# Optimization experiments

Measured on AMD Instinct MI355X. Metric: run time of the kernel, lower is better.

## Reference

```python
import jax, jax.numpy as jnp
import numpy as np

H = 4        # nhead
TEMP = 0.1   # temperature
TOP_K = 5
SHAPE_EPS = 1e-5


def _ln(x, g, b):
    m = x.mean(-1, keepdims=True)
    v = ((x - m) ** 2).mean(-1, keepdims=True)
    return (x - m) / jnp.sqrt(v + SHAPE_EPS) * g + b


def _mha(x, Wqkv, bqkv, Wo, bo):
    B, L, D = x.shape
    Dh = D // H
    qkv = x @ Wqkv.T + bqkv                     # [B,L,3D]
    q, k, v = jnp.split(qkv, 3, axis=-1)
    q = q.reshape(B, L, H, Dh)
    k = k.reshape(B, L, H, Dh)
    v = v.reshape(B, L, H, Dh)
    att = jnp.einsum('bqhd,bkhd->bhqk', q, k) * (1.0 / np.sqrt(Dh))
    att = jax.nn.softmax(att, axis=-1)
    o = jnp.einsum('bhqk,bkhd->bqhd', att, v).reshape(B, L, D)
    return o @ Wo.T + bo


def _pattern_encoder(x, cls_token, Wqkv, bqkv, Wo, bo, ln1_g, ln1_b,
                     W1, b1, W2, b2, ln2_g, ln2_b, proj_W, proj_b, proj_g, proj_bb):
    B, L, D = x.shape
    h = jnp.concatenate([jnp.broadcast_to(cls_token, (B, 1, D)), x], axis=1)  # [B,L+1,D]
    for i in range(Wqkv.shape[0]):  # num_layers=2, post-norm (PyTorch default)
        a = _mha(h, Wqkv[i], bqkv[i], Wo[i], bo[i])
        h = _ln(h + a, ln1_g[i], ln1_b[i])
        f = jax.nn.gelu(h @ W1[i].T + b1[i], approximate=False) @ W2[i].T + b2[i]
        h = _ln(h + f, ln2_g[i], ln2_b[i])
    cls_out = h[:, 0, :]
    return _ln(cls_out @ proj_W.T + proj_b, proj_g, proj_bb)  # [B,d_repr]


def _value_encoder(xm, vW1, vb1, v_g, v_b, vW2, vb2):
    hh = _ln(xm @ vW1.T + vb1, v_g, v_b)
    return jax.nn.gelu(hh, approximate=False) @ vW2.T + vb2


def setup_inputs() -> dict:
    B, L, D, DR, N, P, NL = 64, 512, 512, 128, 10000, 96, 2
    key = jax.random.key(0)
    ks = jax.random.split(key, 16)
    sc = 0.02
    inp = {
        'query': jax.random.normal(ks[0], (B, L, D), jnp.float32),
        'memory_keys': jax.random.normal(ks[1], (N, DR), jnp.float32),
        'memory_values': jax.random.normal(ks[2], (N, P, D), jnp.float32),
        'cls_token': jax.random.normal(ks[3], (1, 1, D), jnp.float32) * sc,
        'Wqkv': jax.random.normal(ks[4], (NL, 3 * D, D), jnp.float32) * sc,
        'bqkv': jnp.zeros((NL, 3 * D), jnp.float32),
        'Wo': jax.random.normal(ks[5], (NL, D, D), jnp.float32) * sc,
        'bo': jnp.zeros((NL, D), jnp.float32),
        'ln1_g': jnp.ones((NL, D), jnp.float32),
        'ln1_b': jnp.zeros((NL, D), jnp.float32),
        'W1': jax.random.normal(ks[6], (NL, 2 * D, D), jnp.float32) * sc,
        'b1': jnp.zeros((NL, 2 * D), jnp.float32),
        'W2': jax.random.normal(ks[7], (NL, D, 2 * D), jnp.float32) * sc,
        'b2': jnp.zeros((NL, D), jnp.float32),
        'ln2_g': jnp.ones((NL, D), jnp.float32),
        'ln2_b': jnp.zeros((NL, D), jnp.float32),
        'proj_W': jax.random.normal(ks[8], (DR, D), jnp.float32) * sc,
        'proj_b': jnp.zeros((DR,), jnp.float32),
        'proj_g': jnp.ones((DR,), jnp.float32),
        'proj_bb': jnp.zeros((DR,), jnp.float32),
        'vW1': jax.random.normal(ks[9], (DR, D), jnp.float32) * sc,
        'vb1': jnp.zeros((DR,), jnp.float32),
        'v_g': jnp.ones((DR,), jnp.float32),
        'v_b': jnp.zeros((DR,), jnp.float32),
        'vW2': jax.random.normal(ks[10], (DR, DR), jnp.float32) * sc,
        'vb2': jnp.zeros((DR,), jnp.float32),
        'shape_w': jnp.float32(0.5),
    }
    return inp


def reference(query, memory_keys, memory_values, cls_token, Wqkv, bqkv, Wo, bo,
              ln1_g, ln1_b, W1, b1, W2, b2, ln2_g, ln2_b,
              proj_W, proj_b, proj_g, proj_bb, vW1, vb1, v_g, v_b, vW2, vb2, shape_w):
    q_repr = _pattern_encoder(query, cls_token, Wqkv, bqkv, Wo, bo, ln1_g, ln1_b,
                              W1, b1, W2, b2, ln2_g, ln2_b, proj_W, proj_b, proj_g, proj_bb)
    q_val = _value_encoder(query.mean(axis=1), vW1, vb1, v_g, v_b, vW2, vb2)
    qk = shape_w * q_repr + (1.0 - shape_w) * q_val              # [B,DR]
    # squared euclidean distance, expanded form (same math as sum((a-b)^2))
    d = ((qk ** 2).sum(-1)[:, None]
         - 2.0 * qk @ memory_keys.T
         + (memory_keys ** 2).sum(-1)[None, :])                  # [B,N]
    sim = -d / TEMP
    top_scores, top_idx = jax.lax.top_k(sim, TOP_K)              # [B,K]
    weights = jax.nn.softmax(top_scores, axis=-1)
    retrieved = memory_values[top_idx]                           # [B,K,P,D]
    return retrieved, weights
```

## Files before the change

### kernel.cpp

```cpp
#include <hip/hip_runtime.h>
#include <math.h>

#define B_    64
#define LQ    512
#define LC    513
#define DD    512
#define HH    4
#define DH    128
#define DRr   128
#define NKEYS 10000
#define PP    96
#define TOPK  5
#define MROWS (B_*LC)
#define VTSTRIDE 544

typedef __attribute__((ext_vector_type(8))) short short8v;
typedef __attribute__((ext_vector_type(4))) float f32x4;
typedef __attribute__((ext_vector_type(16))) float f32x16;

static __device__ __forceinline__ float gelu_exact(float x) {
    return 0.5f * x * (1.0f + erff(x * 0.70710678118654752440f));
}

static __device__ __forceinline__ unsigned short f2bf(float x) {
    union { float f; unsigned u; } v; v.f = x;
    unsigned r = v.u + 0x7fff + ((v.u >> 16) & 1);
    return (unsigned short)(r >> 16);
}
static __device__ __forceinline__ float bf2f(unsigned short h) {
    union { float f; unsigned u; } v; v.u = ((unsigned)h) << 16;
    return v.f;
}
static __device__ __forceinline__ void split_bf(float x, unsigned short& hi, unsigned short& lo) {
    hi = f2bf(x);
    lo = f2bf(x - bf2f(hi));
}

static __device__ __forceinline__ int xcd_swz(int orig, int nwg) {
    int xcd = orig & 7;
    int lid = orig >> 3;
    int q = nwg >> 3, r = nwg & 7;
    int base = (xcd < r) ? xcd * (q + 1) : r * (q + 1) + (xcd - r) * q;
    return base + lid;
}

static __device__ __forceinline__ void gload16(const unsigned short* g, unsigned short* l) {
    __builtin_amdgcn_global_load_lds(
        (const __attribute__((address_space(1))) unsigned*)g,
        (__attribute__((address_space(3))) unsigned*)l, 16, 0, 0);
}

__global__ __launch_bounds__(256)
void split_kernel(const float* __restrict__ x, unsigned short* __restrict__ hi,
                  unsigned short* __restrict__ lo, int n4)
{
    int i = blockIdx.x * blockDim.x + threadIdx.x;
    if (i >= n4) return;
    float4 v = ((const float4*)x)[i];
    unsigned short h0,h1,h2,h3,l0,l1,l2,l3;
    split_bf(v.x,h0,l0); split_bf(v.y,h1,l1); split_bf(v.z,h2,l2); split_bf(v.w,h3,l3);
    ((uint2*)hi)[i] = make_uint2((unsigned)h0 | ((unsigned)h1 << 16), (unsigned)h2 | ((unsigned)h3 << 16));
    ((uint2*)lo)[i] = make_uint2((unsigned)l0 | ((unsigned)l1 << 16), (unsigned)l2 | ((unsigned)l3 << 16));
}

__global__ __launch_bounds__(256)
void concat_cls(const float* __restrict__ query, const float* __restrict__ cls,
                float* __restrict__ h, unsigned short* __restrict__ h_hi,
                unsigned short* __restrict__ h_lo)
{
    int row = blockIdx.x * 4 + (threadIdx.x >> 6);
    int lane = threadIdx.x & 63;
    int b = row / LC, r = row - b * LC;
    const float* src = (r == 0) ? (cls + lane * 8)
                                : (query + ((size_t)b * LQ + (r - 1)) * DD + lane * 8);
    float4 v0 = *(const float4*)src;
    float4 v1 = *(const float4*)(src + 4);
    size_t o = (size_t)row * DD + lane * 8;
    *(float4*)(h + o) = v0;
    *(float4*)(h + o + 4) = v1;
    float vv[8] = {v0.x,v0.y,v0.z,v0.w,v1.x,v1.y,v1.z,v1.w};
    unsigned short hs[8], ls[8];
    #pragma unroll
    for (int i = 0; i < 8; i++) split_bf(vv[i], hs[i], ls[i]);
    uint4 hv, lv;
    hv.x = (unsigned)hs[0] | ((unsigned)hs[1] << 16);
    hv.y = (unsigned)hs[2] | ((unsigned)hs[3] << 16);
    hv.z = (unsigned)hs[4] | ((unsigned)hs[5] << 16);
    hv.w = (unsigned)hs[6] | ((unsigned)hs[7] << 16);
    lv.x = (unsigned)ls[0] | ((unsigned)ls[1] << 16);
    lv.y = (unsigned)ls[2] | ((unsigned)ls[3] << 16);
    lv.z = (unsigned)ls[4] | ((unsigned)ls[5] << 16);
    lv.w = (unsigned)ls[6] | ((unsigned)ls[7] << 16);
    *(uint4*)(h_hi + o) = hv;
    *(uint4*)(h_lo + o) = lv;
}

#define BM 128
#define BN 128
#define BK 32

#define MFMA32(a, b, c) __builtin_amdgcn_mfma_f32_32x32x16_bf16(a, b, c, 0, 0, 0)

template<int MODE>
__global__ __launch_bounds__(256)
void gemm3(const unsigned short* __restrict__ Ahi, const unsigned short* __restrict__ Alo,
           const unsigned short* __restrict__ Whi, const unsigned short* __restrict__ Wlo,
           const float* __restrict__ bias, const float* __restrict__ res,
           float* __restrict__ Cf, unsigned short* __restrict__ Chi,
           unsigned short* __restrict__ Clo, unsigned* __restrict__ Vix,
           int M, int N, int K, int NBN)
{
    __shared__ __align__(16) unsigned short POOL[32768];

    const int t = threadIdx.x;
    const int lane = t & 63, w = t >> 6;
    const int wr = w >> 1, wc = w & 1;
    const int wg = xcd_swz(blockIdx.x, gridDim.x);
    const int bm = wg / NBN, bn = wg - bm * NBN;
    const int row0 = bm * BM, col0 = bn * BN;

    const int srow = t >> 2;
    const int sg   = t & 3;
    const int glog = sg ^ (srow & 3);
    int ar0 = row0 + srow;      if (ar0 >= M) ar0 = M - 1;
    int ar1 = row0 + srow + 64; if (ar1 >= M) ar1 = M - 1;
    const size_t aoff0 = (size_t)ar0 * K + glog * 8;
    const size_t aoff1 = (size_t)ar1 * K + glog * 8;
    const size_t boff0 = (size_t)(col0 + srow) * K + glog * 8;
    const size_t boff1 = (size_t)(col0 + srow + 64) * K + glog * 8;
    const int ldso0 = t * 8;
    const int ldso1 = t * 8 + 2048;

    f32x16 acc[2][2];
    #pragma unroll
    for (int m = 0; m < 2; m++)
        #pragma unroll
        for (int n = 0; n < 2; n++)
            #pragma unroll
            for (int i = 0; i < 16; i++) acc[m][n][i] = 0.f;

    const int cl = lane & 31;
    const int kg = lane >> 5;
    const int cl3 = cl & 3;

    const int KT = K / BK;
    gload16(Ahi + aoff0, &POOL[ldso0]);
    gload16(Ahi + aoff1, &POOL[ldso1]);
    gload16(Alo + aoff0, &POOL[4096 + ldso0]);
    gload16(Alo + aoff1, &POOL[4096 + ldso1]);
    gload16(Whi + boff0, &POOL[8192 + ldso0]);
    gload16(Whi + boff1, &POOL[8192 + ldso1]);
    gload16(Wlo + boff0, &POOL[12288 + ldso0]);
    gload16(Wlo + boff1, &POOL[12288 + ldso1]);

    for (int kt = 0; kt < KT; kt++) {
        const int cb = (kt & 1) * 16384;
        const int nb = 16384 - cb;
        if (kt + 1 < KT) {
            const int k0n = (kt + 1) * BK;
            gload16(Ahi + aoff0 + k0n, &POOL[nb + ldso0]);
            gload16(Ahi + aoff1 + k0n, &POOL[nb + ldso1]);
            gload16(Alo + aoff0 + k0n, &POOL[nb + 4096 + ldso0]);
            gload16(Alo + aoff1 + k0n, &POOL[nb + 4096 + ldso1]);
            gload16(Whi + boff0 + k0n, &POOL[nb + 8192 + ldso0]);
            gload16(Whi + boff1 + k0n, &POOL[nb + 8192 + ldso1]);
            gload16(Wlo + boff0 + k0n, &POOL[nb + 12288 + ldso0]);
            gload16(Wlo + boff1 + k0n, &POOL[nb + 12288 + ldso1]);
            asm volatile("s_waitcnt vmcnt(8)" ::: "memory");
        } else {
            asm volatile("s_waitcnt vmcnt(0)" ::: "memory");
        }
        __builtin_amdgcn_s_barrier();
        __builtin_amdgcn_sched_barrier(0);

        #pragma unroll
        for (int ks = 0; ks < 2; ks++) {
            const int blkswz = ((ks * 2 + kg) ^ cl3) * 8;
            short8v ah[2], al[2], bh[2], bl[2];
            #pragma unroll
            for (int m = 0; m < 2; m++) {
                int off = cb + (wr * 64 + m * 32 + cl) * 32 + blkswz;
                ah[m] = *(const short8v*)&POOL[off];
                al[m] = *(const short8v*)&POOL[off + 4096];
            }
            #pragma unroll
            for (int n = 0; n < 2; n++) {
                int off = cb + (wc * 64 + n * 32 + cl) * 32 + blkswz;
                bh[n] = *(const short8v*)&POOL[off + 8192];
                bl[n] = *(const short8v*)&POOL[off + 12288];
            }
            #pragma unroll
            for (int m = 0; m < 2; m++)
                #pragma unroll
                for (int n = 0; n < 2; n++) {
                    acc[m][n] = MFMA32(ah[m], bh[n], acc[m][n]);
                    acc[m][n] = MFMA32(al[m], bh[n], acc[m][n]);
                    acc[m][n] = MFMA32(ah[m], bl[n], acc[m][n]);
                }
        }
        __builtin_amdgcn_s_barrier();
    }

    if (MODE == 3 && col0 >= 1024) {
        const int hh = (col0 - 1024) >> 7;
        unsigned* VS = (unsigned*)POOL;
        const int bb0 = row0 / LC;
        const int bound = (bb0 + 1) * LC;
        const int ddl = t >> 3, j0 = (t & 7) * 16;
        #pragma unroll
        for (int p = 0; p < 4; p++) {
            __syncthreads();
            if (wc == (p >> 1)) {
                const int ccl = col0 + wc * 64 + (p & 1) * 32 + cl;
                const float bcol = bias[ccl];
                #pragma unroll
                for (int m = 0; m < 2; m++) {
                    const int lrb = wr * 64 + m * 32 + 4 * kg;
                    #pragma unroll
                    for (int q = 0; q < 4; q++)
                        #pragma unroll
                        for (int r = 0; r < 4; r++) {
                            float v = ((p & 1) ? acc[m][1][q * 4 + r]
                                               : acc[m][0][q * 4 + r]) + bcol;
                            unsigned short hv, lv;
                            split_bf(v, hv, lv);
                            VS[cl * 129 + lrb + 8 * q + r] =
                                (unsigned)hv | ((unsigned)lv << 16);
                        }
                }
            }
            __syncthreads();
            long long vb0 = (long long)((bb0 * HH + hh) * DH + p * 32 + ddl) * VTSTRIDE
                            - (long long)bb0 * LC;
            long long vb1 = (long long)(((bb0 + 1) * HH + hh) * DH + p * 32 + ddl) * VTSTRIDE
                            - (long long)(bb0 + 1) * LC;
            #pragma unroll
            for (int j = 0; j < 16; j++) {
                int row = row0 + j0 + j;
                if (row < M) {
                    long long vi = (row < bound ? vb0 : vb1) + row;
                    Vix[vi] = VS[ddl * 129 + j0 + j];
                }
            }
        }
        return;
    }

    #pragma unroll
    for (int m = 0; m < 2; m++) {
        const int rb = row0 + wr * 64 + m * 32 + 4 * kg;
        #pragma unroll
        for (int n = 0; n < 2; n++) {
            const int cc = col0 + wc * 64 + n * 32 + cl;
            const float bcol = bias[cc];
            #pragma unroll
            for (int q = 0; q < 4; q++) {
                #pragma unroll
                for (int r = 0; r < 4; r++) {
                    int row = rb + 8 * q + r;
                    if (row < M) {
                        float v = acc[m][n][q * 4 + r] + bcol;
                        if (MODE == 1) v += res[(size_t)row * N + cc];
                        if (MODE == 2) {
                            v = gelu_exact(v);
                            unsigned short hv, lv;
                            split_bf(v, hv, lv);
                            Chi[(size_t)row * N + cc] = hv;
                            Clo[(size_t)row * N + cc] = lv;
                        } else if (MODE == 3) {
                            unsigned short hv, lv;
                            split_bf(v, hv, lv);
                            Chi[(size_t)row * 1024 + cc] = hv;
                            Clo[(size_t)row * 1024 + cc] = lv;
                        } else {
                            Cf[(size_t)row * N + cc] = v;
                        }
                    }
                }
            }
        }
    }
}

#define AQT 64
#define AKT 32
#define NKT2 17
#define MFMA16(a, b, c) __builtin_amdgcn_mfma_f32_16x16x32_bf16(a, b, c, 0, 0, 0)
__global__ __launch_bounds__(256)
void attn_mfma(const unsigned short* __restrict__ qkhi, const unsigned short* __restrict__ qklo,
               const unsigned* __restrict__ vtx,
               unsigned short* __restrict__ ohi, unsigned short* __restrict__ olo)
{
    __shared__ __align__(16) unsigned short SM[24064];
    #define KH(r,d) SM[(r)*136 + (d)]
    #define KL(r,d) SM[4352 + (r)*136 + (d)]
    #define VH(d,k) SM[8704 + (d)*40 + (k)]
    #define VL(d,k) SM[13824 + (d)*40 + (k)]
    #define PH(r,k) SM[18944 + (r)*40 + (k)]
    #define PL(r,k) SM[21504 + (r)*40 + (k)]
    #define OS(r,d) SM[(r)*136 + (d)]

    const int t = threadIdx.x;
    const int lane = t & 63, w = t >> 6;
    const int id = xcd_swz(blockIdx.x, gridDim.x);
    const int qt = id % 9;
    const int hb = id / 9;
    const int h = hb & 3, b = hb >> 2;
    const int q0 = qt * AQT;
    const int c = lane & 15, g = lane >> 4;
    const float SCALE = 0.08838834764831845f;

    short8v qh[4], ql[4];
    {
        int qrow = b * LC + q0 + w * 16 + c;
        if (qrow > MROWS - 1) qrow = MROWS - 1;
        const unsigned short* bh_ = qkhi + (size_t)qrow * 1024 + h * DH;
        const unsigned short* bl_ = qklo + (size_t)qrow * 1024 + h * DH;
        #pragma unroll
        for (int ks = 0; ks < 4; ks++) {
            qh[ks] = *(const short8v*)(bh_ + ks * 32 + g * 8);
            ql[ks] = *(const short8v*)(bl_ + ks * 32 + g * 8);
        }
    }

    float m_r[4], l_r[4];
    #pragma unroll
    for (int r = 0; r < 4; r++) { m_r[r] = -INFINITY; l_r[r] = 0.f; }
    f32x4 acc_o[8];
    #pragma unroll
    for (int n = 0; n < 8; n++) { acc_o[n][0]=0.f; acc_o[n][1]=0.f; acc_o[n][2]=0.f; acc_o[n][3]=0.f; }

    const int skr = t >> 3, skd = (t & 7) * 16;
    const int svd = t >> 1, svk = (t & 1) * 16;
    const unsigned short* kbase  = qkhi + 512 + h * DH + skd;
    const unsigned short* kbasel = qklo + 512 + h * DH + skd;
    const unsigned* vbase = vtx + ((size_t)((b * HH + h) * DH + svd)) * VTSTRIDE + svk;

    short8v rk0, rk1, rl0, rl1;
    uint4 rv0, rv1, rv2, rv3;
    {
        int krow = b * LC + skr; if (krow > MROWS - 1) krow = MROWS - 1;
        const unsigned short* kb  = kbase  + (size_t)krow * 1024;
        const unsigned short* kbl = kbasel + (size_t)krow * 1024;
        rk0 = *(const short8v*)kb;  rk1 = *(const short8v*)(kb + 8);
        rl0 = *(const short8v*)kbl; rl1 = *(const short8v*)(kbl + 8);
        rv0 = *(const uint4*)(vbase);
        rv1 = *(const uint4*)(vbase + 4);
        rv2 = *(const uint4*)(vbase + 8);
        rv3 = *(const uint4*)(vbase + 12);
    }

    for (int kt = 0; kt < NKT2; kt++) {
        __builtin_amdgcn_s_barrier();
        *(short8v*)&KH(skr, skd)     = rk0;
        *(short8v*)&KH(skr, skd + 8) = rk1;
        *(short8v*)&KL(skr, skd)     = rl0;
        *(short8v*)&KL(skr, skd + 8) = rl1;
        {
            uint4 hA, hB, lA, lB;
            hA.x = (rv0.x & 0xffffu) | (rv0.y << 16);
            hA.y = (rv0.z & 0xffffu) | (rv0.w << 16);
            hA.z = (rv1.x & 0xffffu) | (rv1.y << 16);
            hA.w = (rv1.z & 0xffffu) | (rv1.w << 16);
            hB.x = (rv2.x & 0xffffu) | (rv2.y << 16);
            hB.y = (rv2.z & 0xffffu) | (rv2.w << 16);
            hB.z = (rv3.x & 0xffffu) | (rv3.y << 16);
            hB.w = (rv3.z & 0xffffu) | (rv3.w << 16);
            lA.x = (rv0.x >> 16) | (rv0.y & 0xffff0000u);
            lA.y = (rv0.z >> 16) | (rv0.w & 0xffff0000u);
            lA.z = (rv1.x >> 16) | (rv1.y & 0xffff0000u);
            lA.w = (rv1.z >> 16) | (rv1.w & 0xffff0000u);
            lB.x = (rv2.x >> 16) | (rv2.y & 0xffff0000u);
            lB.y = (rv2.z >> 16) | (rv2.w & 0xffff0000u);
            lB.z = (rv3.x >> 16) | (rv3.y & 0xffff0000u);
            lB.w = (rv3.z >> 16) | (rv3.w & 0xffff0000u);
            *(uint4*)&VH(svd, svk)     = hA;
            *(uint4*)&VH(svd, svk + 8) = hB;
            *(uint4*)&VL(svd, svk)     = lA;
            *(uint4*)&VL(svd, svk + 8) = lB;
        }
        if (kt + 1 < NKT2) {
            int krow = b * LC + (kt + 1) * AKT + skr;
            if (krow > MROWS - 1) krow = MROWS - 1;
            const unsigned short* kb  = kbase  + (size_t)krow * 1024;
            const unsigned short* kbl = kbasel + (size_t)krow * 1024;
            rk0 = *(const short8v*)kb;  rk1 = *(const short8v*)(kb + 8);
            rl0 = *(const short8v*)kbl; rl1 = *(const short8v*)(kbl + 8);
            const unsigned* vb = vbase + (kt + 1) * AKT;
            rv0 = *(const uint4*)(vb);
            rv1 = *(const uint4*)(vb + 4);
            rv2 = *(const uint4*)(vb + 8);
            rv3 = *(const uint4*)(vb + 12);
        }
        asm volatile("s_waitcnt lgkmcnt(0)" ::: "memory");
        __builtin_amdgcn_s_barrier();
        __builtin_amdgcn_sched_barrier(0);

        f32x4 s[2];
        s[0][0]=s[0][1]=s[0][2]=s[0][3]=0.f;
        s[1][0]=s[1][1]=s[1][2]=s[1][3]=0.f;
        __builtin_amdgcn_s_setprio(1);
        #pragma unroll
        for (int n = 0; n < 2; n++) {
            #pragma unroll
            for (int ks = 0; ks < 4; ks++) {
                short8v kh = *(const short8v*)&KH(n * 16 + c, ks * 32 + g * 8);
                short8v kl = *(const short8v*)&KL(n * 16 + c, ks * 32 + g * 8);
                s[n] = MFMA16(qh[ks], kh, s[n]);
                s[n] = MFMA16(ql[ks], kh, s[n]);
                s[n] = MFMA16(qh[ks], kl, s[n]);
            }
        }
        __builtin_amdgcn_s_setprio(0);

        #pragma unroll
        for (int n = 0; n < 2; n++) {
            bool oob = (kt * 32 + n * 16 + c) >= LC;
            #pragma unroll
            for (int r = 0; r < 4; r++) {
                float sv = s[n][r] * SCALE;
                s[n][r] = oob ? -INFINITY : sv;
            }
        }

        float alpha[4], p0v[4], p1v[4];
        #pragma unroll
        for (int r = 0; r < 4; r++) {
            float rm = fmaxf(s[0][r], s[1][r]);
            #pragma unroll
            for (int off = 1; off < 16; off <<= 1) rm = fmaxf(rm, __shfl_xor(rm, off));
            float mn = fmaxf(m_r[r], rm);
            float p0 = expf(s[0][r] - mn);
            float p1 = expf(s[1][r] - mn);
            float ts = p0 + p1;
            #pragma unroll
            for (int off = 1; off < 16; off <<= 1) ts += __shfl_xor(ts, off);
            float al = expf(m_r[r] - mn);
            m_r[r] = mn;
            l_r[r] = al * l_r[r] + ts;
            alpha[r] = al;
            p0v[r] = p0; p1v[r] = p1;
        }

        #pragma unroll
        for (int n = 0; n < 8; n++)
            #pragma unroll
            for (int r = 0; r < 4; r++) acc_o[n][r] *= alpha[r];

        #pragma unroll
        for (int r = 0; r < 4; r++) {
            unsigned short ph, pl;
            split_bf(p0v[r], ph, pl);
            PH(w * 16 + g * 4 + r, c) = ph;
            PL(w * 16 + g * 4 + r, c) = pl;
            split_bf(p1v[r], ph, pl);
            PH(w * 16 + g * 4 + r, 16 + c) = ph;
            PL(w * 16 + g * 4 + r, 16 + c) = pl;
        }
        short8v pah = *(const short8v*)&PH(w * 16 + c, g * 8);
        short8v pal = *(const short8v*)&PL(w * 16 + c, g * 8);
        __builtin_amdgcn_s_setprio(1);
        #pragma unroll
        for (int n = 0; n < 8; n++) {
            short8v vh = *(const short8v*)&VH(n * 16 + c, g * 8);
            short8v vl = *(const short8v*)&VL(n * 16 + c, g * 8);
            acc_o[n] = MFMA16(pah, vh, acc_o[n]);
            acc_o[n] = MFMA16(pal, vh, acc_o[n]);
            acc_o[n] = MFMA16(pah, vl, acc_o[n]);
        }
        __builtin_amdgcn_s_setprio(0);
    }

    float inv[4];
    #pragma unroll
    for (int r = 0; r < 4; r++) inv[r] = 1.0f / l_r[r];

    const int orow = t >> 2, oc0 = (t & 3) * 32;
    #pragma unroll
    for (int pass = 0; pass < 2; pass++) {
        __syncthreads();
        #pragma unroll
        for (int n = 0; n < 8; n++)
            #pragma unroll
            for (int r = 0; r < 4; r++) {
                float v = acc_o[n][r] * inv[r];
                unsigned short hv, lv;
                split_bf(v, hv, lv);
                OS(w * 16 + g * 4 + r, n * 16 + c) = pass ? lv : hv;
            }
        __syncthreads();
        int grow = q0 + orow;
        if (grow < LC) {
            unsigned short* dst = (pass ? olo : ohi) + ((size_t)(b * LC + grow)) * DD + h * DH + oc0;
            #pragma unroll
            for (int u = 0; u < 4; u++)
                *(short8v*)(dst + u * 8) = *(const short8v*)&OS(orow, oc0 + u * 8);
        }
    }
    #undef KH
    #undef KL
    #undef VH
    #undef VL
    #undef PH
    #undef PL
    #undef OS
}

__global__ __launch_bounds__(256)
void ln512(const float* __restrict__ X, const float* __restrict__ g,
           const float* __restrict__ bb, float* __restrict__ Y,
           unsigned short* __restrict__ Yhi, unsigned short* __restrict__ Ylo)
{
    int row = blockIdx.x * 4 + (threadIdx.x >> 6);
    int lane = threadIdx.x & 63;
    const float* x = X + (size_t)row * DD + lane * 8;
    float4 v0 = *(const float4*)x;
    float4 v1 = *(const float4*)(x + 4);
    float vv[8] = {v0.x,v0.y,v0.z,v0.w,v1.x,v1.y,v1.z,v1.w};
    float s = 0.f;
    #pragma unroll
    for (int i = 0; i < 8; i++) s += vv[i];
    #pragma unroll
    for (int off = 1; off < 64; off <<= 1) s += __shfl_xor(s, off);
    float mean = s * (1.0f / 512.0f);
    float d[8], s2 = 0.f;
    #pragma unroll
    for (int i = 0; i < 8; i++) { d[i] = vv[i] - mean; s2 += d[i] * d[i]; }
    #pragma unroll
    for (int off = 1; off < 64; off <<= 1) s2 += __shfl_xor(s2, off);
    float var = s2 * (1.0f / 512.0f);
    float rstd = 1.0f / sqrtf(var + 1e-5f);
    float4 g0 = *(const float4*)(g + lane * 8);
    float4 g1 = *(const float4*)(g + lane * 8 + 4);
    float4 b0 = *(const float4*)(bb + lane * 8);
    float4 b1 = *(const float4*)(bb + lane * 8 + 4);
    float gg[8] = {g0.x,g0.y,g0.z,g0.w,g1.x,g1.y,g1.z,g1.w};
    float bv[8] = {b0.x,b0.y,b0.z,b0.w,b1.x,b1.y,b1.z,b1.w};
    float ov[8];
    unsigned short hs[8], ls[8];
    #pragma unroll
    for (int i = 0; i < 8; i++) {
        ov[i] = d[i] * rstd * gg[i] + bv[i];
        split_bf(ov[i], hs[i], ls[i]);
    }
    size_t o = (size_t)row * DD + lane * 8;
    *(float4*)(Y + o)     = make_float4(ov[0], ov[1], ov[2], ov[3]);
    *(float4*)(Y + o + 4) = make_float4(ov[4], ov[5], ov[6], ov[7]);
    uint4 hv, lv;
    hv.x = (unsigned)hs[0] | ((unsigned)hs[1] << 16);
    hv.y = (unsigned)hs[2] | ((unsigned)hs[3] << 16);
    hv.z = (unsigned)hs[4] | ((unsigned)hs[5] << 16);
    hv.w = (unsigned)hs[6] | ((unsigned)hs[7] << 16);
    lv.x = (unsigned)ls[0] | ((unsigned)ls[1] << 16);
    lv.y = (unsigned)ls[2] | ((unsigned)ls[3] << 16);
    lv.z = (unsigned)ls[4] | ((unsigned)ls[5] << 16);
    lv.w = (unsigned)ls[6] | ((unsigned)ls[7] << 16);
    *(uint4*)(Yhi + o) = hv;
    *(uint4*)(Ylo + o) = lv;
}

__global__ __launch_bounds__(128)
void mean_part(const float* __restrict__ query, float* __restrict__ part)
{
    int b = blockIdx.x, ch = blockIdx.y, t = threadIdx.x;
    const float* base = query + ((size_t)b * LQ + ch * 64) * DD + t * 4;
    float ax = 0.f, ay = 0.f, az = 0.f, aw = 0.f;
    for (int l = 0; l < 64; l++) {
        float4 v = *(const float4*)(base + (size_t)l * DD);
        ax += v.x; ay += v.y; az += v.z; aw += v.w;
    }
    *(float4*)(part + ((size_t)(b * 8 + ch)) * DD + t * 4) = make_float4(ax, ay, az, aw);
}

__global__ __launch_bounds__(128)
void mean_fin(const float* __restrict__ part, float* __restrict__ xm)
{
    int b = blockIdx.x, t = threadIdx.x;
    float ax = 0.f, ay = 0.f, az = 0.f, aw = 0.f;
    #pragma unroll
    for (int ch = 0; ch < 8; ch++) {
        float4 v = *(const float4*)(part + ((size_t)(b * 8 + ch)) * DD + t * 4);
        ax += v.x; ay += v.y; az += v.z; aw += v.w;
    }
    *(float4*)(xm + (size_t)b * DD + t * 4) =
        make_float4(ax * (1.f/512.f), ay * (1.f/512.f), az * (1.f/512.f), aw * (1.f/512.f));
}

static __device__ __forceinline__ float block128_sum(float x, float* red, int t) {
    #pragma unroll
    for (int off = 1; off < 64; off <<= 1) x += __shfl_xor(x, off);
    if ((t & 63) == 0) red[t >> 6] = x;
    __syncthreads();
    float r = red[0] + red[1];
    __syncthreads();
    return r;
}

__global__ __launch_bounds__(128)
void proj_ln(const float* __restrict__ h, const float* __restrict__ pW, const float* __restrict__ pb,
             const float* __restrict__ pg, const float* __restrict__ pbb, float* __restrict__ q_repr)
{
    __shared__ float xs[DD];
    __shared__ float red[2];
    int b = blockIdx.x, t = threadIdx.x;
    *(float4*)&xs[t * 4] = *(const float4*)(h + (size_t)(b * LC) * DD + t * 4);
    __syncthreads();
    const float* w = pW + (size_t)t * DD;
    float acc = pb[t];
    for (int k = 0; k < DD; k += 4) {
        float4 a = *(const float4*)&xs[k];
        float4 ww = *(const float4*)(w + k);
        acc += a.x * ww.x + a.y * ww.y + a.z * ww.z + a.w * ww.w;
    }
    float mean = block128_sum(acc, red, t) * (1.f / 128.f);
    float dx = acc - mean;
    float var = block128_sum(dx * dx, red, t) * (1.f / 128.f);
    float rstd = 1.0f / sqrtf(var + 1e-5f);
    q_repr[(size_t)b * DRr + t] = dx * rstd * pg[t] + pbb[t];
}

__global__ __launch_bounds__(128)
void venc(const float* __restrict__ xm, const float* __restrict__ vW1, const float* __restrict__ vb1,
          const float* __restrict__ vg, const float* __restrict__ vb,
          const float* __restrict__ vW2, const float* __restrict__ vb2,
          float* __restrict__ q_val)
{
    __shared__ float xs[DD];
    __shared__ float hg[DRr];
    __shared__ float red[2];
    int b = blockIdx.x, t = threadIdx.x;
    *(float4*)&xs[t * 4] = *(const float4*)(xm + (size_t)b * DD + t * 4);
    __syncthreads();
    const float* w = vW1 + (size_t)t * DD;
    float acc = vb1[t];
    for (int k = 0; k < DD; k += 4) {
        float4 a = *(const float4*)&xs[k];
        float4 ww = *(const float4*)(w + k);
        acc += a.x * ww.x + a.y * ww.y + a.z * ww.z + a.w * ww.w;
    }
    float mean = block128_sum(acc, red, t) * (1.f / 128.f);
    float dx = acc - mean;
    float var = block128_sum(dx * dx, red, t) * (1.f / 128.f);
    float rstd = 1.0f / sqrtf(var + 1e-5f);
    float hn = dx * rstd * vg[t] + vb[t];
    hg[t] = gelu_exact(hn);
    __syncthreads();
    const float* w2 = vW2 + (size_t)t * DRr;
    float acc2 = vb2[t];
    for (int k = 0; k < DRr; k += 4) {
        float4 a = *(const float4*)&hg[k];
        float4 ww = *(const float4*)(w2 + k);
        acc2 += a.x * ww.x + a.y * ww.y + a.z * ww.z + a.w * ww.w;
    }
    q_val[(size_t)b * DRr + t] = acc2;
}

__global__ void combine_qk(const float* __restrict__ qr, const float* __restrict__ qv,
                           const float* __restrict__ swp, float* __restrict__ qk)
{
    int i = blockIdx.x * blockDim.x + threadIdx.x;
    if (i < B_ * DRr) {
        float sw = swp[0];
        qk[i] = sw * qr[i] + (1.f - sw) * qv[i];
    }
}

#define SIMCH 10
__global__ __launch_bounds__(256)
void sim_kernel(const float* __restrict__ qk, const float* __restrict__ mkeys, float* __restrict__ sim)
{
    __shared__ float qs[DRr];
    int b = blockIdx.x, ch = blockIdx.y, t = threadIdx.x;
    if (t < DRr) qs[t] = qk[(size_t)b * DRr + t];
    __syncthreads();
    float qn = 0.f;
    #pragma unroll 8
    for (int i = 0; i < DRr; i++) qn += qs[i] * qs[i];
    int n0 = ch * (NKEYS / SIMCH), n1 = n0 + (NKEYS / SIMCH);
    for (int n = n0 + t; n < n1; n += 256) {
        const float* kr = mkeys + (size_t)n * DRr;
        float dot = 0.f, kn = 0.f;
        #pragma unroll 8
        for (int i = 0; i < DRr; i += 4) {
            float4 kv = *(const float4*)(kr + i);
            dot += qs[i] * kv.x + qs[i + 1] * kv.y + qs[i + 2] * kv.z + qs[i + 3] * kv.w;
            kn  += kv.x * kv.x + kv.y * kv.y + kv.z * kv.z + kv.w * kv.w;
        }
        float d = qn - 2.f * dot + kn;
        sim[(size_t)b * NKEYS + n] = -d / 0.1f;
    }
}

static __device__ __forceinline__ void topk_insert(float* v, int* id, float x, int n) {
    bool better = (x > v[TOPK - 1]) || (x == v[TOPK - 1] && n < id[TOPK - 1]);
    if (better) {
        v[TOPK - 1] = x; id[TOPK - 1] = n;
        #pragma unroll
        for (int k = TOPK - 1; k > 0; k--) {
            bool sw = (v[k] > v[k - 1]) || (v[k] == v[k - 1] && id[k] < id[k - 1]);
            if (!sw) break;
            float tv = v[k]; v[k] = v[k - 1]; v[k - 1] = tv;
            int ti = id[k]; id[k] = id[k - 1]; id[k - 1] = ti;
        }
    }
}

__global__ __launch_bounds__(256)
void topk_kernel(const float* __restrict__ sim, int* __restrict__ topidx, float* __restrict__ wout)
{
    __shared__ float sv[256][TOPK];
    __shared__ int   si[256][TOPK];
    int b = blockIdx.x, t = threadIdx.x;
    float v[TOPK]; int id[TOPK];
    #pragma unroll
    for (int k = 0; k < TOPK; k++) { v[k] = -INFINITY; id[k] = 0x7fffffff; }
    for (int n = t; n < NKEYS; n += 256) {
        topk_insert(v, id, sim[(size_t)b * NKEYS + n], n);
    }
    #pragma unroll
    for (int k = 0; k < TOPK; k++) { sv[t][k] = v[k]; si[t][k] = id[k]; }
    for (int strd = 128; strd >= 1; strd >>= 1) {
        __syncthreads();
        if (t < strd) {
            #pragma unroll
            for (int k = 0; k < TOPK; k++) topk_insert(v, id, sv[t + strd][k], si[t + strd][k]);
            #pragma unroll
            for (int k = 0; k < TOPK; k++) { sv[t][k] = v[k]; si[t][k] = id[k]; }
        }
    }
    if (t == 0) {
        float m = v[0];
        float e[TOPK]; float sum = 0.f;
        #pragma unroll
        for (int k = 0; k < TOPK; k++) { e[k] = expf(v[k] - m); sum += e[k]; }
        #pragma unroll
        for (int k = 0; k < TOPK; k++) {
            wout[(size_t)b * TOPK + k] = e[k] / sum;
            topidx[b * TOPK + k] = id[k];
        }
    }
}

__global__ __launch_bounds__(128)
void gather_kernel(const float* __restrict__ mv, const int* __restrict__ topidx, float* __restrict__ out)
{
    int blk = blockIdx.x;
    int b = blk / (TOPK * PP);
    int rem = blk - b * (TOPK * PP);
    int k = rem / PP;
    int p = rem - k * PP;
    int idx = topidx[b * TOPK + k];
    const float4* src = (const float4*)(mv + ((size_t)idx * PP + p) * DD);
    float4* dst = (float4*)(out + (size_t)blk * DD);
    dst[threadIdx.x] = src[threadIdx.x];
}

extern "C" void kernel_launch(void* const* d_in, const int* in_sizes, int n_in,
                              void* d_out, int out_size, void* d_ws, size_t ws_size,
                              hipStream_t stream) {
    const float* query = (const float*)d_in[0];
    const float* mkeys = (const float*)d_in[1];
    const float* mvals = (const float*)d_in[2];
    const float* cls   = (const float*)d_in[3];
    const float* Wqkv  = (const float*)d_in[4];
    const float* bqkv  = (const float*)d_in[5];
    const float* Wo    = (const float*)d_in[6];
    const float* bo    = (const float*)d_in[7];
    const float* ln1g  = (const float*)d_in[8];
    const float* ln1b  = (const float*)d_in[9];
    const float* W1    = (const float*)d_in[10];
    const float* b1    = (const float*)d_in[11];
    const float* W2    = (const float*)d_in[12];
    const float* b2    = (const float*)d_in[13];
    const float* ln2g  = (const float*)d_in[14];
    const float* ln2b  = (const float*)d_in[15];
    const float* pW    = (const float*)d_in[16];
    const float* pb    = (const float*)d_in[17];
    const float* pg    = (const float*)d_in[18];
    const float* pbb   = (const float*)d_in[19];
    const float* vW1   = (const float*)d_in[20];
    const float* vb1   = (const float*)d_in[21];
    const float* vg    = (const float*)d_in[22];
    const float* vb    = (const float*)d_in[23];
    const float* vW2   = (const float*)d_in[24];
    const float* vb2   = (const float*)d_in[25];
    const float* swp   = (const float*)d_in[26];
    float* out = (float*)d_out;

    float* ws    = (float*)d_ws;
    float* h     = ws;
    float* preln = h + (size_t)MROWS * DD;
    unsigned short* h_hi  = (unsigned short*)(preln + (size_t)MROWS * DD);
    unsigned short* h_lo  = h_hi  + (size_t)MROWS * DD;
    unsigned short* mid_hi = h_lo + (size_t)MROWS * DD;
    unsigned short* mid_lo = mid_hi + (size_t)MROWS * 1024;
    unsigned short* qkhi  = mid_lo + (size_t)MROWS * 1024;
    unsigned short* qklo  = qkhi  + (size_t)MROWS * 1024;
    unsigned* vtx         = (unsigned*)(qklo + (size_t)MROWS * 1024);
    unsigned short* wq_hi = (unsigned short*)(vtx + (size_t)32768 * VTSTRIDE);
    unsigned short* wq_lo = wq_hi + (size_t)2 * 1536 * DD;
    unsigned short* wo_hi = wq_lo + (size_t)2 * 1536 * DD;
    unsigned short* wo_lo = wo_hi + (size_t)2 * DD * DD;
    unsigned short* w1_hi = wo_lo + (size_t)2 * DD * DD;
    unsigned short* w1_lo = w1_hi + (size_t)2 * 1024 * DD;
    unsigned short* w2_hi = w1_lo + (size_t)2 * 1024 * DD;
    unsigned short* w2_lo = w2_hi + (size_t)2 * DD * 1024;
    float* xm   = (float*)(w2_lo + (size_t)2 * DD * 1024);
    float* qval = xm   + (size_t)B_ * DD;
    float* qrep = qval + (size_t)B_ * DRr;
    float* qkc  = qrep + (size_t)B_ * DRr;
    float* simb = qkc  + (size_t)B_ * DRr;
    int*   tidx = (int*)(simb + (size_t)B_ * NKEYS);
    float* mpart = (float*)(tidx + 512);
    (void)ws_size; (void)in_sizes; (void)n_in; (void)out_size;

    {
        int n4;
        n4 = 2 * 1536 * DD / 4;
        split_kernel<<<(n4 + 255) / 256, 256, 0, stream>>>(Wqkv, wq_hi, wq_lo, n4);
        n4 = 2 * DD * DD / 4;
        split_kernel<<<(n4 + 255) / 256, 256, 0, stream>>>(Wo, wo_hi, wo_lo, n4);
        n4 = 2 * 1024 * DD / 4;
        split_kernel<<<(n4 + 255) / 256, 256, 0, stream>>>(W1, w1_hi, w1_lo, n4);
        n4 = 2 * DD * 1024 / 4;
        split_kernel<<<(n4 + 255) / 256, 256, 0, stream>>>(W2, w2_hi, w2_lo, n4);
    }

    concat_cls<<<MROWS / 4, 256, 0, stream>>>(query, cls, h, h_hi, h_lo);

    for (int l = 0; l < 2; l++) {
        const unsigned short* wqh = wq_hi + (size_t)l * 1536 * DD;
        const unsigned short* wql = wq_lo + (size_t)l * 1536 * DD;
        const unsigned short* woh = wo_hi + (size_t)l * DD * DD;
        const unsigned short* wol = wo_lo + (size_t)l * DD * DD;
        const unsigned short* w1h = w1_hi + (size_t)l * 1024 * DD;
        const unsigned short* w1l = w1_lo + (size_t)l * 1024 * DD;
        const unsigned short* w2h = w2_hi + (size_t)l * DD * 1024;
        const unsigned short* w2l = w2_lo + (size_t)l * DD * 1024;
        const float* bq  = bqkv + (size_t)l * 1536;
        const float* bol = bo   + (size_t)l * DD;
        const float* g1  = ln1g + (size_t)l * DD;
        const float* be1 = ln1b + (size_t)l * DD;
        const float* b1l = b1   + (size_t)l * 1024;
        const float* b2l = b2   + (size_t)l * DD;
        const float* g2  = ln2g + (size_t)l * DD;
        const float* be2 = ln2b + (size_t)l * DD;

        gemm3<3><<<257 * 12, 256, 0, stream>>>(h_hi, h_lo, wqh, wql, bq, nullptr,
                                               nullptr, qkhi, qklo, vtx,
                                               MROWS, 1536, DD, 12);
        attn_mfma<<<9 * HH * B_, 256, 0, stream>>>(qkhi, qklo, vtx, h_hi, h_lo);
        gemm3<1><<<257 * 4, 256, 0, stream>>>(h_hi, h_lo, woh, wol, bol, h,
                                              preln, nullptr, nullptr, nullptr,
                                              MROWS, DD, DD, 4);
        ln512<<<MROWS / 4, 256, 0, stream>>>(preln, g1, be1, h, h_hi, h_lo);
        gemm3<2><<<257 * 8, 256, 0, stream>>>(h_hi, h_lo, w1h, w1l, b1l, nullptr,
                                              nullptr, mid_hi, mid_lo, nullptr,
                                              MROWS, 1024, DD, 8);
        gemm3<1><<<257 * 4, 256, 0, stream>>>(mid_hi, mid_lo, w2h, w2l, b2l, h,
                                              preln, nullptr, nullptr, nullptr,
                                              MROWS, DD, 1024, 4);
        ln512<<<MROWS / 4, 256, 0, stream>>>(preln, g2, be2, h, h_hi, h_lo);
    }

    proj_ln<<<B_, 128, 0, stream>>>(h, pW, pb, pg, pbb, qrep);
    mean_part<<<dim3(B_, 8), 128, 0, stream>>>(query, mpart);
    mean_fin<<<B_, 128, 0, stream>>>(mpart, xm);
    venc<<<B_, 128, 0, stream>>>(xm, vW1, vb1, vg, vb, vW2, vb2, qval);
    combine_qk<<<(B_ * DRr + 255) / 256, 256, 0, stream>>>(qrep, qval, swp, qkc);
    sim_kernel<<<dim3(B_, SIMCH), 256, 0, stream>>>(qkc, mkeys, simb);
    topk_kernel<<<B_, 256, 0, stream>>>(simb, tidx, out + (size_t)B_ * TOPK * PP * DD);
    gather_kernel<<<B_ * TOPK * PP, 128, 0, stream>>>(mvals, tidx, out);
}
```

Measured before the change: 2.490 ms.

## Widen GEMM tiles to 128x256 with single-buffered LDS and 4x2 warp tiles

The split-bf16 GEMM output tile grows from 128x128 to 128x256. Each warp now owns all 128 rows and a 64-column slice, so it holds 4x2 accumulators, and grid sizes are halved to match. The LDS double buffer and its async prefetch pipeline are dropped in favour of a single buffer guarded by syncthreads around each load, which cuts LDS so that two blocks can share a CU (launch_bounds 256,2). The aim is more operand reuse per loaded byte and fewer A-matrix reloads, at the cost of global-load latency no longer overlapping MFMA work and higher register pressure.

```diff
diff --git a/kernel.cpp b/kernel.cpp
--- a/kernel.cpp
+++ b/kernel.cpp
@@ -96,13 +96,13 @@
 }
 
 #define BM 128
-#define BN 128
+#define BN 256
 #define BK 32
 
 #define MFMA32(a, b, c) __builtin_amdgcn_mfma_f32_32x32x16_bf16(a, b, c, 0, 0, 0)
 
 template<int MODE>
-__global__ __launch_bounds__(256)
+__global__ __launch_bounds__(256, 2)
 void gemm3(const unsigned short* __restrict__ Ahi, const unsigned short* __restrict__ Alo,
            const unsigned short* __restrict__ Whi, const unsigned short* __restrict__ Wlo,
            const float* __restrict__ bias, const float* __restrict__ res,
@@ -110,30 +110,37 @@
            unsigned short* __restrict__ Clo, unsigned* __restrict__ Vix,
            int M, int N, int K, int NBN)
 {
-    __shared__ __align__(16) unsigned short POOL[32768];
+    __shared__ __align__(16) unsigned short POOL[24576];
 
     const int t = threadIdx.x;
     const int lane = t & 63, w = t >> 6;
-    const int wr = w >> 1, wc = w & 1;
     const int wg = xcd_swz(blockIdx.x, gridDim.x);
     const int bm = wg / NBN, bn = wg - bm * NBN;
     const int row0 = bm * BM, col0 = bn * BN;
 
-    const int srow = t >> 2;
-    const int sg   = t & 3;
-    const int glog = sg ^ (srow & 3);
-    int ar0 = row0 + srow;      if (ar0 >= M) ar0 = M - 1;
-    int ar1 = row0 + srow + 64; if (ar1 >= M) ar1 = M - 1;
-    const size_t aoff0 = (size_t)ar0 * K + glog * 8;
-    const size_t aoff1 = (size_t)ar1 * K + glog * 8;
-    const size_t boff0 = (size_t)(col0 + srow) * K + glog * 8;
-    const size_t boff1 = (size_t)(col0 + srow + 64) * K + glog * 8;
-    const int ldso0 = t * 8;
-    const int ldso1 = t * 8 + 2048;
-
-    f32x16 acc[2][2];
-    #pragma unroll
-    for (int m = 0; m < 2; m++)
+    size_t aofs[2]; int aldo[2];
+    size_t bofs[4]; int bldo[4];
+    #pragma unroll
+    for (int j = 0; j < 2; j++) {
+        int p = w * 128 + j * 64 + lane;
+        int row = p >> 2, sg = p & 3;
+        int glog = sg ^ (row & 3);
+        int ar = row0 + row; if (ar >= M) ar = M - 1;
+        aofs[j] = (size_t)ar * K + glog * 8;
+        aldo[j] = p * 8;
+    }
+    #pragma unroll
+    for (int j = 0; j < 4; j++) {
+        int p = w * 256 + j * 64 + lane;
+        int row = p >> 2, sg = p & 3;
+        int glog = sg ^ (row & 3);
+        bofs[j] = (size_t)(col0 + row) * K + glog * 8;
+        bldo[j] = p * 8;
+    }
+
+    f32x16 acc[4][2];
+    #pragma unroll
+    for (int m = 0; m < 4; m++)
         #pragma unroll
         for (int n = 0; n < 2; n++)
             #pragma unroll
@@ -144,53 +151,39 @@
     const int cl3 = cl & 3;
 
     const int KT = K / BK;
-    gload16(Ahi + aoff0, &POOL[ldso0]);
-    gload16(Ahi + aoff1, &POOL[ldso1]);
-    gload16(Alo + aoff0, &POOL[4096 + ldso0]);
-    gload16(Alo + aoff1, &POOL[4096 + ldso1]);
-    gload16(Whi + boff0, &POOL[8192 + ldso0]);
-    gload16(Whi + boff1, &POOL[8192 + ldso1]);
-    gload16(Wlo + boff0, &POOL[12288 + ldso0]);
-    gload16(Wlo + boff1, &POOL[12288 + ldso1]);
-
     for (int kt = 0; kt < KT; kt++) {
-        const int cb = (kt & 1) * 16384;
-        const int nb = 16384 - cb;
-        if (kt + 1 < KT) {
-            const int k0n = (kt + 1) * BK;
-            gload16(Ahi + aoff0 + k0n, &POOL[nb + ldso0]);
-            gload16(Ahi + aoff1 + k0n, &POOL[nb + ldso1]);
-            gload16(Alo + aoff0 + k0n, &POOL[nb + 4096 + ldso0]);
-            gload16(Alo + aoff1 + k0n, &POOL[nb + 4096 + ldso1]);
-            gload16(Whi + boff0 + k0n, &POOL[nb + 8192 + ldso0]);
-            gload16(Whi + boff1 + k0n, &POOL[nb + 8192 + ldso1]);
-            gload16(Wlo + boff0 + k0n, &POOL[nb + 12288 + ldso0]);
-            gload16(Wlo + boff1 + k0n, &POOL[nb + 12288 + ldso1]);
-            asm volatile("s_waitcnt vmcnt(8)" ::: "memory");
-        } else {
-            asm volatile("s_waitcnt vmcnt(0)" ::: "memory");
-        }
-        __builtin_amdgcn_s_barrier();
-        __builtin_amdgcn_sched_barrier(0);
+        const int k0 = kt * BK;
+        __syncthreads();
+        #pragma unroll
+        for (int j = 0; j < 2; j++) {
+            gload16(Ahi + aofs[j] + k0, &POOL[aldo[j]]);
+            gload16(Alo + aofs[j] + k0, &POOL[4096 + aldo[j]]);
+        }
+        #pragma unroll
+        for (int j = 0; j < 4; j++) {
+            gload16(Whi + bofs[j] + k0, &POOL[8192 + bldo[j]]);
+            gload16(Wlo + bofs[j] + k0, &POOL[16384 + bldo[j]]);
+        }
+        __syncthreads();
 
         #pragma unroll
         for (int ks = 0; ks < 2; ks++) {
             const int blkswz = ((ks * 2 + kg) ^ cl3) * 8;
-            short8v ah[2], al[2], bh[2], bl[2];
-            #pragma unroll
-            for (int m = 0; m < 2; m++) {
-                int off = cb + (wr * 64 + m * 32 + cl) * 32 + blkswz;
+            short8v ah[4], al[4], bh[2], bl[2];
+            #pragma unroll
+            for (int m = 0; m < 4; m++) {
+                int off = (m * 32 + cl) * 32 + blkswz;
                 ah[m] = *(const short8v*)&POOL[off];
                 al[m] = *(const short8v*)&POOL[off + 4096];
             }
             #pragma unroll
             for (int n = 0; n < 2; n++) {
-                int off = cb + (wc * 64 + n * 32 + cl) * 32 + blkswz;
-                bh[n] = *(const short8v*)&POOL[off + 8192];
-                bl[n] = *(const short8v*)&POOL[off + 12288];
+                int off = (w * 64 + n * 32 + cl) * 32 + blkswz;
+                bh[n] = *(const short8v*)&POOL[8192 + off];
+                bl[n] = *(const short8v*)&POOL[16384 + off];
             }
             #pragma unroll
-            for (int m = 0; m < 2; m++)
+            for (int m = 0; m < 4; m++)
                 #pragma unroll
                 for (int n = 0; n < 2; n++) {
                     acc[m][n] = MFMA32(ah[m], bh[n], acc[m][n]);
@@ -198,30 +191,28 @@
                     acc[m][n] = MFMA32(ah[m], bl[n], acc[m][n]);
                 }
         }
-        __builtin_amdgcn_s_barrier();
     }
 
     if (MODE == 3 && col0 >= 1024) {
-        const int hh = (col0 - 1024) >> 7;
         unsigned* VS = (unsigned*)POOL;
         const int bb0 = row0 / LC;
         const int bound = (bb0 + 1) * LC;
         const int ddl = t >> 3, j0 = (t & 7) * 16;
         #pragma unroll
-        for (int p = 0; p < 4; p++) {
+        for (int p = 0; p < 8; p++) {
             __syncthreads();
-            if (wc == (p >> 1)) {
-                const int ccl = col0 + wc * 64 + (p & 1) * 32 + cl;
-                const float bcol = bias[ccl];
+            if (w == (p >> 1)) {
+                const int n = p & 1;
+                const float bcol = bias[col0 + p * 32 + cl];
                 #pragma unroll
-                for (int m = 0; m < 2; m++) {
-                    const int lrb = wr * 64 + m * 32 + 4 * kg;
+                for (int m = 0; m < 4; m++) {
+                    const int lrb = m * 32 + 4 * kg;
                     #pragma unroll
                     for (int q = 0; q < 4; q++)
                         #pragma unroll
                         for (int r = 0; r < 4; r++) {
-                            float v = ((p & 1) ? acc[m][1][q * 4 + r]
-                                               : acc[m][0][q * 4 + r]) + bcol;
+                            float v = ((n) ? acc[m][1][q * 4 + r]
+                                           : acc[m][0][q * 4 + r]) + bcol;
                             unsigned short hv, lv;
                             split_bf(v, hv, lv);
                             VS[cl * 129 + lrb + 8 * q + r] =
@@ -230,9 +221,11 @@
                 }
             }
             __syncthreads();
-            long long vb0 = (long long)((bb0 * HH + hh) * DH + p * 32 + ddl) * VTSTRIDE
+            int dglob = col0 - 1024 + p * 32 + ddl;
+            int hh = dglob >> 7, dd = dglob & 127;
+            long long vb0 = (long long)((bb0 * HH + hh) * DH + dd) * VTSTRIDE
                             - (long long)bb0 * LC;
-            long long vb1 = (long long)(((bb0 + 1) * HH + hh) * DH + p * 32 + ddl) * VTSTRIDE
+            long long vb1 = (long long)(((bb0 + 1) * HH + hh) * DH + dd) * VTSTRIDE
                             - (long long)(bb0 + 1) * LC;
             #pragma unroll
             for (int j = 0; j < 16; j++) {
@@ -247,11 +240,11 @@
     }
 
     #pragma unroll
-    for (int m = 0; m < 2; m++) {
-        const int rb = row0 + wr * 64 + m * 32 + 4 * kg;
+    for (int m = 0; m < 4; m++) {
+        const int rb = row0 + m * 32 + 4 * kg;
         #pragma unroll
         for (int n = 0; n < 2; n++) {
-            const int cc = col0 + wc * 64 + n * 32 + cl;
+            const int cc = col0 + w * 64 + n * 32 + cl;
             const float bcol = bias[cc];
             #pragma unroll
             for (int q = 0; q < 4; q++) {
@@ -846,20 +839,20 @@
         const float* g2  = ln2g + (size_t)l * DD;
         const float* be2 = ln2b + (size_t)l * DD;
 
-        gemm3<3><<<257 * 12, 256, 0, stream>>>(h_hi, h_lo, wqh, wql, bq, nullptr,
-                                               nullptr, qkhi, qklo, vtx,
-                                               MROWS, 1536, DD, 12);
+        gemm3<3><<<257 * 6, 256, 0, stream>>>(h_hi, h_lo, wqh, wql, bq, nullptr,
+                                              nullptr, qkhi, qklo, vtx,
+                                              MROWS, 1536, DD, 6);
         attn_mfma<<<9 * HH * B_, 256, 0, stream>>>(qkhi, qklo, vtx, h_hi, h_lo);
-        gemm3<1><<<257 * 4, 256, 0, stream>>>(h_hi, h_lo, woh, wol, bol, h,
+        gemm3<1><<<257 * 2, 256, 0, stream>>>(h_hi, h_lo, woh, wol, bol, h,
                                               preln, nullptr, nullptr, nullptr,
-                                              MROWS, DD, DD, 4);
+                                              MROWS, DD, DD, 2);
         ln512<<<MROWS / 4, 256, 0, stream>>>(preln, g1, be1, h, h_hi, h_lo);
-        gemm3<2><<<257 * 8, 256, 0, stream>>>(h_hi, h_lo, w1h, w1l, b1l, nullptr,
+        gemm3<2><<<257 * 4, 256, 0, stream>>>(h_hi, h_lo, w1h, w1l, b1l, nullptr,
                                               nullptr, mid_hi, mid_lo, nullptr,
-                                              MROWS, 1024, DD, 8);
-        gemm3<1><<<257 * 4, 256, 0, stream>>>(mid_hi, mid_lo, w2h, w2l, b2l, h,
+                                              MROWS, 1024, DD, 4);
+        gemm3<1><<<257 * 2, 256, 0, stream>>>(mid_hi, mid_lo, w2h, w2l, b2l, h,
                                               preln, nullptr, nullptr, nullptr,
-                                              MROWS, DD, 1024, 4);
+                                              MROWS, DD, 1024, 2);
         ln512<<<MROWS / 4, 256, 0, stream>>>(preln, g2, be2, h, h_hi, h_lo);
     }
 
```

Result: slower. 2.810 ms (+12.9%).

## Replace double-buffered LDS prefetch with single-buffered load-sync-compute loop in gemm3

Applied to the files above, without the earlier changes.

The GEMM main loop no longer prefetches the next K-tile into a second LDS buffer while computing the current one. Each iteration now syncs, loads the tile into a single buffer, syncs again and computes. This halves the shared-memory pool, which may allow more resident blocks per CU. In exchange it gives up the overlap of global loads with MFMA work and adds a second barrier per iteration. The epilogue that reuses the pool may also depend on its original size.

```diff
diff --git a/kernel.cpp b/kernel.cpp
--- a/kernel.cpp
+++ b/kernel.cpp
@@ -110,7 +110,7 @@
            unsigned short* __restrict__ Clo, unsigned* __restrict__ Vix,
            int M, int N, int K, int NBN)
 {
-    __shared__ __align__(16) unsigned short POOL[32768];
+    __shared__ __align__(16) unsigned short POOL[16384];
 
     const int t = threadIdx.x;
     const int lane = t & 63, w = t >> 6;
@@ -143,35 +143,24 @@
     const int kg = lane >> 5;
     const int cl3 = cl & 3;
 
+    unsigned short* LAh = POOL;
+    unsigned short* LAl = POOL + 4096;
+    unsigned short* LBh = POOL + 8192;
+    unsigned short* LBl = POOL + 12288;
+
     const int KT = K / BK;
-    gload16(Ahi + aoff0, &POOL[ldso0]);
-    gload16(Ahi + aoff1, &POOL[ldso1]);
-    gload16(Alo + aoff0, &POOL[4096 + ldso0]);
-    gload16(Alo + aoff1, &POOL[4096 + ldso1]);
-    gload16(Whi + boff0, &POOL[8192 + ldso0]);
-    gload16(Whi + boff1, &POOL[8192 + ldso1]);
-    gload16(Wlo + boff0, &POOL[12288 + ldso0]);
-    gload16(Wlo + boff1, &POOL[12288 + ldso1]);
-
     for (int kt = 0; kt < KT; kt++) {
-        const int cb = (kt & 1) * 16384;
-        const int nb = 16384 - cb;
-        if (kt + 1 < KT) {
-            const int k0n = (kt + 1) * BK;
-            gload16(Ahi + aoff0 + k0n, &POOL[nb + ldso0]);
-            gload16(Ahi + aoff1 + k0n, &POOL[nb + ldso1]);
-            gload16(Alo + aoff0 + k0n, &POOL[nb + 4096 + ldso0]);
-            gload16(Alo + aoff1 + k0n, &POOL[nb + 4096 + ldso1]);
-            gload16(Whi + boff0 + k0n, &POOL[nb + 8192 + ldso0]);
-            gload16(Whi + boff1 + k0n, &POOL[nb + 8192 + ldso1]);
-            gload16(Wlo + boff0 + k0n, &POOL[nb + 12288 + ldso0]);
-            gload16(Wlo + boff1 + k0n, &POOL[nb + 12288 + ldso1]);
-            asm volatile("s_waitcnt vmcnt(8)" ::: "memory");
-        } else {
-            asm volatile("s_waitcnt vmcnt(0)" ::: "memory");
-        }
-        __builtin_amdgcn_s_barrier();
-        __builtin_amdgcn_sched_barrier(0);
+        const int k0 = kt * BK;
+        __syncthreads();
+        gload16(Ahi + aoff0 + k0, &LAh[ldso0]);
+        gload16(Ahi + aoff1 + k0, &LAh[ldso1]);
+        gload16(Alo + aoff0 + k0, &LAl[ldso0]);
+        gload16(Alo + aoff1 + k0, &LAl[ldso1]);
+        gload16(Whi + boff0 + k0, &LBh[ldso0]);
+        gload16(Whi + boff1 + k0, &LBh[ldso1]);
+        gload16(Wlo + boff0 + k0, &LBl[ldso0]);
+        gload16(Wlo + boff1 + k0, &LBl[ldso1]);
+        __syncthreads();
 
         #pragma unroll
         for (int ks = 0; ks < 2; ks++) {
@@ -179,15 +168,15 @@
             short8v ah[2], al[2], bh[2], bl[2];
             #pragma unroll
             for (int m = 0; m < 2; m++) {
-                int off = cb + (wr * 64 + m * 32 + cl) * 32 + blkswz;
-                ah[m] = *(const short8v*)&POOL[off];
-                al[m] = *(const short8v*)&POOL[off + 4096];
+                int off = (wr * 64 + m * 32 + cl) * 32 + blkswz;
+                ah[m] = *(const short8v*)&LAh[off];
+                al[m] = *(const short8v*)&LAl[off];
             }
             #pragma unroll
             for (int n = 0; n < 2; n++) {
-                int off = cb + (wc * 64 + n * 32 + cl) * 32 + blkswz;
-                bh[n] = *(const short8v*)&POOL[off + 8192];
-                bl[n] = *(const short8v*)&POOL[off + 12288];
+                int off = (wc * 64 + n * 32 + cl) * 32 + blkswz;
+                bh[n] = *(const short8v*)&LBh[off];
+                bl[n] = *(const short8v*)&LBl[off];
             }
             #pragma unroll
             for (int m = 0; m < 2; m++)
@@ -198,7 +187,6 @@
                     acc[m][n] = MFMA32(ah[m], bl[n], acc[m][n]);
                 }
         }
-        __builtin_amdgcn_s_barrier();
     }
 
     if (MODE == 3 && col0 >= 1024) {
```

After: 2.421 ms, median of 2. 1.03x faster.
